# Kernel tuning notes

Measured on AMD Instinct MI355X. Metric: run time of the kernel, lower is better.

Reference implementation:

```python
import jax, jax.numpy as jnp
import numpy as np

N_CLASSES = 10   # number of distinct private-attribute labels
DIM = 16         # PCA / GMM dimension (init arg `dim`)
SIGMA = 1.0      # init arg `sigma`, cov = sigma * I


def _pca(X, k):
    # torch PCA: center, SVD of X^T, project onto first k left singular vectors
    X = X - jnp.mean(X, axis=0)
    U, _, _ = jnp.linalg.svd(X.T, full_matrices=False)  # U: [D, min(D,B)]
    return X @ U[:, :k]                                  # [B, k]


def _gmm_loss(x, labels):
    # x: [B, k] PCA-projected features, labels: [B] int class ids in [0, C)
    B = x.shape[0]
    dtype = x.dtype
    ones = jnp.ones((B,), dtype)
    counts = jax.ops.segment_sum(ones, labels, num_segments=N_CLASSES)          # [C]
    sums = jax.ops.segment_sum(x, labels, num_segments=N_CLASSES)               # [C, k]
    safe = jnp.maximum(counts, 1.0)
    means = sums / safe[:, None]                                                # [C, k]

    diff = x - means[labels]                                                    # [B, k]
    outers = diff[:, :, None] * diff[:, None, :]                                # [B, k, k]
    Ssum = jax.ops.segment_sum(outers, labels, num_segments=N_CLASSES)          # [C, k, k]
    Sigma = SIGMA * jnp.eye(DIM, dtype=dtype) + Ssum / safe[:, None, None]      # [C, k, k]

    inv = jnp.linalg.inv(Sigma)                                                 # [C, k, k]
    _, logdet = jnp.linalg.slogdet(Sigma)                                       # [C]

    # KL(N_i || N_j) = 0.5*(tr(S_j^-1 S_i) + (u_j-u_i)^T S_j^-1 (u_j-u_i) - k + logdet_j - logdet_i)
    tr = jnp.einsum('jab,iba->ij', inv, Sigma)                                  # [C, C]
    d = means[None, :, :] - means[:, None, :]                                   # d[i,j] = u_j - u_i
    maha = jnp.einsum('ija,jab,ijb->ij', d, inv, d)                             # [C, C]
    kl = 0.5 * (tr + maha - DIM + logdet[None, :] - logdet[:, None])            # [C, C]

    present = counts > 0
    W = counts[:, None] * counts[None, :]
    mask = present[:, None] & present[None, :] & ~jnp.eye(N_CLASSES, dtype=bool)
    result = jnp.sum(jnp.where(mask, kl * W, jnp.zeros_like(kl)))
    return result / (jnp.asarray(B, dtype) ** 3)


def setup_inputs() -> dict:
    key = jax.random.key(0)
    k1, k2 = jax.random.split(key)
    mu = jax.random.normal(k1, (16384, 1024), dtype=jnp.float32)
    private_attribute = jax.random.randint(k2, (16384,), 0, N_CLASSES, dtype=jnp.int32)
    return {"mu": mu, "private_attribute": private_attribute}


def reference(mu, private_attribute):
    B = mu.shape[0]
    x = mu.reshape(B, -1)          # flatten(start_dim=1)
    x = _pca(x, DIM)               # [B, DIM]
    labels = private_attribute.astype(jnp.int32)
    return _gmm_loss(x, labels)
```

## Files before the change

### kernel.cpp

```cpp
#include <hip/hip_runtime.h>
#include <math.h>

#define BN 16384
#define DN 1024

static constexpr size_t OFF_C    = 0x000000;
static constexpr size_t OFF_P    = 0x400000;
static constexpr size_t OFF_Y0   = 0x800000;
static constexpr size_t OFF_Y1   = 0x840000;
static constexpr size_t OFF_Y2   = 0x880000;
static constexpr size_t OFF_Y3   = 0x8C0000;
static constexpr size_t OFF_CQ   = 0x900000;
static constexpr size_t OFF_S64  = 0x940000;
static constexpr size_t OFF_LF   = 0x948000;
static constexpr size_t OFF_T64  = 0x950000;
static constexpr size_t OFF_V16  = 0x958000;
static constexpr size_t OFF_UT   = 0x960000;
static constexpr size_t OFF_UTT  = 0x970000;
static constexpr size_t OFF_S16  = 0x980000;
static constexpr size_t OFF_CS   = 0x980100;
static constexpr size_t OFF_TR   = 0x981100;
static constexpr size_t OFF_SCAL = 0x981200;
static constexpr size_t OFF_STAT = 0x981300;
static constexpr size_t OFF_F    = 0x990000;
static constexpr size_t OFF_M    = 0xA90000;

typedef float f32x4 __attribute__((ext_vector_type(4)));
typedef short bf16x8 __attribute__((ext_vector_type(8)));
typedef unsigned int u32x4v __attribute__((ext_vector_type(4)));

__device__ __forceinline__ float wsumf(float v){
  #pragma unroll
  for (int off=32; off; off>>=1) v += __shfl_xor(v, off, 64);
  return v;
}
__device__ __forceinline__ float wminf(float v){
  #pragma unroll
  for (int off=32; off; off>>=1) v = fminf(v, __shfl_xor(v, off, 64));
  return v;
}
__device__ __forceinline__ float wmaxf(float v){
  #pragma unroll
  for (int off=32; off; off>>=1) v = fmaxf(v, __shfl_xor(v, off, 64));
  return v;
}
__device__ __forceinline__ float lanebc(float x, int l){
  return __int_as_float(__builtin_amdgcn_readlane(__float_as_int(x), l));
}
__device__ __forceinline__ float wred64(float x){
  x += __int_as_float(__builtin_amdgcn_update_dpp(0, __float_as_int(x), 0x118, 0xf, 0xf, true));
  x += __int_as_float(__builtin_amdgcn_update_dpp(0, __float_as_int(x), 0x114, 0xf, 0xf, true));
  x += __int_as_float(__builtin_amdgcn_update_dpp(0, __float_as_int(x), 0x112, 0xf, 0xf, true));
  x += __int_as_float(__builtin_amdgcn_update_dpp(0, __float_as_int(x), 0x111, 0xf, 0xf, true));
  float s0 = lanebc(x, 15), s1 = lanebc(x, 31), s2 = lanebc(x, 47), s3 = lanebc(x, 63);
  return (s0 + s1) + (s2 + s3);
}


__global__ __launch_bounds__(256) void colsum_k(const float* __restrict__ X, float* __restrict__ cs){
  int b = blockIdx.x, t = threadIdx.x;
  float a0=0.f,a1=0.f,a2=0.f,a3=0.f;
  for (int r=0; r<256; ++r){
    const float4 v = *(const float4*)(X + (size_t)(b*256 + r)*1024 + t*4);
    a0 += v.x; a1 += v.y; a2 += v.z; a3 += v.w;
  }
  atomicAdd(&cs[t*4+0], a0); atomicAdd(&cs[t*4+1], a1);
  atomicAdd(&cs[t*4+2], a2); atomicAdd(&cs[t*4+3], a3);
}

#define SYRK_SLICES 27
#define SYRK_KCHUNK 608
#define SYRKM_SLICES 4
#define SYRKM_KCHUNK 256

__device__ __forceinline__ f32x4 mfma32(bf16x8 a, bf16x8 b, f32x4 c){
  return __builtin_amdgcn_mfma_f32_16x16x32_bf16(a, b, c, 0, 0, 0);
}

template<int KCHUNK>
__device__ __forceinline__ void syrk_mfma_body(const float* __restrict__ X, float* __restrict__ G, int KMAX){
  int bx = blockIdx.x;
  int tp = bx % 36, ks = bx / 36;
  int ti = 0, rem = tp;
  while (rem >= 8 - ti){ rem -= 8 - ti; ++ti; }
  int tj = ti + rem;
  int k0 = ks * KCHUNK;
  int kend = k0 + KCHUNK; if (kend > KMAX) kend = KMAX;

  __shared__ __attribute__((aligned(16))) unsigned int LdsT[2][3][128][20];

  int t = threadIdx.x;
  int wid = t >> 6, lane = t & 63;
  int wr = wid >> 1, wc = wid & 1;
  int lm = lane & 15;
  int lk = lane >> 4;

  f32x4 acc[4][4];
  #pragma unroll
  for (int i=0;i<4;++i)
    #pragma unroll
    for (int j=0;j<4;++j) acc[i][j] = (f32x4){0.f,0.f,0.f,0.f};

  for (int kc = k0; kc < kend; kc += 32){
    __syncthreads();
    #pragma unroll
    for (int w=0; w<4; ++w){
      int job = t + 256*w;
      int c   = job & 127;
      int pk  = job >> 7;
      int p   = pk >> 2;
      int kpg = pk & 3;
      const float* src = X + (size_t)(kc + kpg*8)*1024 + (p ? tj : ti)*128 + c;
      float e[8];
      #pragma unroll
      for (int i=0;i<8;++i) e[i] = src[(size_t)i*1024];
      unsigned hh[8]; float r2f[8]; unsigned mm[8];
      #pragma unroll
      for (int i=0;i<8;++i){
        unsigned u = __float_as_uint(e[i]);
        hh[i] = u & 0xFFFF0000u;
        float r1 = e[i] - __uint_as_float(hh[i]);
        mm[i] = __float_as_uint(r1) & 0xFFFF0000u;
        r2f[i] = r1 - __uint_as_float(mm[i]);
      }
      u32x4v hp, mp, lp;
      #pragma unroll
      for (int j=0;j<4;++j){
        hp[j] = (hh[2*j] >> 16) | hh[2*j+1];
        mp[j] = (mm[2*j] >> 16) | mm[2*j+1];
        lp[j] = (__float_as_uint(r2f[2*j]) >> 16) | (__float_as_uint(r2f[2*j+1]) & 0xFFFF0000u);
      }
      *(u32x4v*)&LdsT[p][0][c][kpg*4] = hp;
      *(u32x4v*)&LdsT[p][1][c][kpg*4] = mp;
      *(u32x4v*)&LdsT[p][2][c][kpg*4] = lp;
    }
    __syncthreads();
    bf16x8 af[3][4], bg[3][4];
    #pragma unroll
    for (int fm=0; fm<4; ++fm){
      int ca = wr*64 + fm*16 + lm;
      int cb = wc*64 + fm*16 + lm;
      #pragma unroll
      for (int tm=0; tm<3; ++tm){
        af[tm][fm] = *(const bf16x8*)&LdsT[0][tm][ca][lk*4];
        bg[tm][fm] = *(const bf16x8*)&LdsT[1][tm][cb][lk*4];
      }
    }
    #pragma unroll
    for (int fm=0; fm<4; ++fm)
      #pragma unroll
      for (int fn=0; fn<4; ++fn){
        f32x4 a = acc[fm][fn];
        a = mfma32(af[0][fm], bg[0][fn], a);
        a = mfma32(af[0][fm], bg[1][fn], a);
        a = mfma32(af[1][fm], bg[0][fn], a);
        a = mfma32(af[0][fm], bg[2][fn], a);
        a = mfma32(af[2][fm], bg[0][fn], a);
        a = mfma32(af[1][fm], bg[1][fn], a);
        acc[fm][fn] = a;
      }
  }
  #pragma unroll
  for (int fm=0; fm<4; ++fm){
    int gi = ti*128 + wr*64 + fm*16 + lk*4;
    #pragma unroll
    for (int fn=0; fn<4; ++fn){
      int gj = tj*128 + wc*64 + fn*16 + lm;
      #pragma unroll
      for (int rg=0; rg<4; ++rg)
        atomicAdd(&G[(size_t)(gi+rg)*1024 + gj], acc[fm][fn][rg]);
    }
  }
}

__global__ __launch_bounds__(256, 2) void syrk_mfma_k(const float* __restrict__ X, float* __restrict__ G){
  syrk_mfma_body<SYRK_KCHUNK>(X, G, 16384);
}
__global__ __launch_bounds__(256, 2) void syrkM_mfma_k(const float* __restrict__ X, float* __restrict__ G){
  syrk_mfma_body<SYRKM_KCHUNK>(X, G, 1024);
}

__global__ __launch_bounds__(256) void trace_k(const float* __restrict__ G, const float* __restrict__ cs,
                                               float* __restrict__ scal){
  __shared__ float red[4];
  int t = threadIdx.x;
  float s = 0.f;
  #pragma unroll
  for (int w=0; w<4; ++w){
    int i = t + 256*w;
    float d = cs[i];
    s += G[(size_t)i*1025] - d*d*(1.0f/16384.0f);
  }
  s = wsumf(s);
  if ((t & 63) == 0) red[t >> 6] = s;
  __syncthreads();
  if (t == 0){
    float trD = (red[0]+red[1]+red[2]+red[3]) * (1.0f/1024.0f);
    float c = 1.40f * trD, a = 0.25f * trD;
    scal[0] = 0.5f*(c + a);
    scal[1] = 2.0f/(c - a);
  }
}

__global__ __launch_bounds__(256) void formCChat_k(float* __restrict__ C, const float* __restrict__ cs,
                                                   const float* __restrict__ scal){
  int g = blockIdx.x*256 + threadIdx.x;
  int i = g >> 10, j = g & 1023;
  if (j < i) return;
  float mid = scal[0], ie = scal[1];
  float v = C[g] - cs[i]*cs[j]*(1.0f/16384.0f);
  float h = ie*(v - ((i==j) ? mid : 0.f));
  C[g] = h;
  C[j*1024 + i] = h;
}

__global__ __launch_bounds__(256) void formM_k(float* __restrict__ M){
  int g = blockIdx.x*256 + threadIdx.x;
  int i = g >> 10, j = g & 1023;
  if (j < i) return;
  float v = 2.f*M[g] - ((i==j) ? 1.f : 0.f);
  M[g] = v;
  M[j*1024 + i] = v;
}

__global__ void rng_k(float* __restrict__ Y){
  int idx = blockIdx.x*256 + threadIdx.x;
  unsigned h = (unsigned)idx * 2654435761u;
  h ^= h >> 16; h *= 2246822519u; h ^= h >> 13; h *= 3266489917u; h ^= h >> 16;
  Y[idx] = (float)(h & 0xFFFFFFu) * (2.0f/16777216.0f) - 1.0f;
}

__global__ __launch_bounds__(256) void mv_k(const float* __restrict__ Yt, const float* __restrict__ Cm, float* __restrict__ P){
  int bx = blockIdx.x;
  int nt = bx & 15, ks = bx >> 4;
  int n0 = nt*64, k0 = ks*64;
  __shared__ __attribute__((aligned(16))) float At[64][68];
  __shared__ __attribute__((aligned(16))) float Bt[64][68];
  int t = threadIdx.x;
  #pragma unroll
  for (int w=0; w<4; ++w){
    int job = t + 256*w;
    int m  = job >> 4, f4 = job & 15;
    float4 v = *(const float4*)(Yt + (size_t)m*1024 + k0 + f4*4);
    At[f4*4+0][m] = v.x; At[f4*4+1][m] = v.y; At[f4*4+2][m] = v.z; At[f4*4+3][m] = v.w;
    int kk = job >> 4, fn = job & 15;
    *(float4*)&Bt[kk][fn*4] = *(const float4*)(Cm + (size_t)(k0+kk)*1024 + n0 + fn*4);
  }
  __syncthreads();
  int tm = t & 15, tn = t >> 4;
  float acc[4][4];
  #pragma unroll
  for (int i=0;i<4;++i)
    #pragma unroll
    for (int j=0;j<4;++j) acc[i][j]=0.f;
  for (int kk=0; kk<64; ++kk){
    float4 a = *(const float4*)&At[kk][tm*4];
    float4 b = *(const float4*)&Bt[kk][tn*4];
    float av[4] = {a.x,a.y,a.z,a.w};
    float bv[4] = {b.x,b.y,b.z,b.w};
    #pragma unroll
    for (int i=0;i<4;++i)
      #pragma unroll
      for (int j=0;j<4;++j) acc[i][j] += av[i]*bv[j];
  }
  #pragma unroll
  for (int i=0;i<4;++i){
    float4 o; o.x=acc[i][0]; o.y=acc[i][1]; o.z=acc[i][2]; o.w=acc[i][3];
    *(float4*)(P + (size_t)(ks*64 + tm*4 + i)*1024 + n0 + tn*4) = o;
  }
}

__global__ __launch_bounds__(256) void combine_k(const float* __restrict__ P, const float* __restrict__ Tk1,
                                                 float* __restrict__ out, int mode){
  int idx = (blockIdx.x*256 + threadIdx.x)*4;
  float s0=0.f,s1=0.f,s2=0.f,s3=0.f;
  #pragma unroll
  for (int ks=0; ks<16; ++ks){
    const float4 p = *(const float4*)(P + (size_t)ks*65536 + idx);
    s0 += p.x; s1 += p.y; s2 += p.z; s3 += p.w;
  }
  float4 o;
  if (mode == 0){
    o.x=s0; o.y=s1; o.z=s2; o.w=s3;
  } else {
    const float4 t1 = *(const float4*)(Tk1 + idx);
    o.x = 2.f*s0 - t1.x; o.y = 2.f*s1 - t1.y;
    o.z = 2.f*s2 - t1.z; o.w = 2.f*s3 - t1.w;
  }
  *(float4*)(out+idx) = o;
}

__global__ __launch_bounds__(256) void gram_k(const float* __restrict__ A, const float* __restrict__ Bm, double* __restrict__ S){
  int bx = blockIdx.x;
  int i = bx >> 2, jg = bx & 3;
  __shared__ __attribute__((aligned(16))) float Ai[1024];
  __shared__ double red[16][17];
  int t = threadIdx.x;
  ((float4*)Ai)[t] = ((const float4*)(A + (size_t)i*1024))[t];
  __syncthreads();
  int jl = t >> 4, kp = t & 15;
  const float* Br = Bm + (size_t)(jg*16 + jl)*1024 + kp*64;
  const float* Ar = Ai + kp*64;
  double acc = 0.0;
  #pragma unroll 8
  for (int kk=0; kk<64; ++kk) acc += (double)Br[kk] * (double)Ar[kk];
  red[jl][kp] = acc;
  __syncthreads();
  if (t < 16){
    double s = 0.0;
    #pragma unroll
    for (int p2=0; p2<16; ++p2) s += red[t][p2];
    S[i*64 + jg*16 + t] = s;
  }
}

__global__ __launch_bounds__(64) void chol_k(const double* __restrict__ S, float* __restrict__ Lf){
  __shared__ double L[64][65];
  __shared__ double col[64];
  int t = threadIdx.x;
  for (int e=t; e<4096; e+=64) L[e>>6][e&63] = S[e];
  __syncthreads();
  for (int k=0; k<64; ++k){
    double lkk = sqrt(fmax(L[k][k], 1e-280));
    double r = 1.0/lkk;
    double ck = (t > k) ? L[t][k]*r : 0.0;
    col[t] = ck;
    if (t == k) L[k][k] = lkk;
    if (t > k)  L[t][k] = ck;
    __syncthreads();
    #pragma unroll
    for (int j=0; j<64; j+=8){
      L[t][j+0] -= ck*col[j+0];
      L[t][j+1] -= ck*col[j+1];
      L[t][j+2] -= ck*col[j+2];
      L[t][j+3] -= ck*col[j+3];
      L[t][j+4] -= ck*col[j+4];
      L[t][j+5] -= ck*col[j+5];
      L[t][j+6] -= ck*col[j+6];
      L[t][j+7] -= ck*col[j+7];
    }
    __syncthreads();
  }
  for (int e=t; e<4096; e+=64){
    int i = e >> 6, j = e & 63;
    Lf[e] = (j < i) ? (float)L[i][j] : ((j == i) ? (float)(1.0/L[i][i]) : 0.f);
  }
}

__global__ __launch_bounds__(256) void applysolve_k(const float* __restrict__ Yin, const float* __restrict__ Lf, float* __restrict__ Qout){
  int k = blockIdx.x*256 + threadIdx.x;
  float z[64];
  #pragma unroll
  for (int c=0; c<64; ++c){
    float v = Yin[(size_t)c*1024 + k];
    #pragma unroll
    for (int j=0; j<c; ++j) v -= Lf[c*64+j]*z[j];
    z[c] = v * Lf[c*64+c];
  }
  #pragma unroll
  for (int c=0; c<64; ++c) Qout[(size_t)c*1024 + k] = z[c];
}

__global__ __launch_bounds__(256) void eig16_k(const double* __restrict__ Tin, float* __restrict__ V16){
  __shared__ float A[64][65];
  __shared__ __attribute__((aligned(16))) float vS[64];
  __shared__ __attribute__((aligned(16))) float qS[64];
  __shared__ float dF[64], eF[64], e2F[64], kapS[64];
  __shared__ float lamF[16];
  __shared__ float IV[5][64][16];
  __shared__ float W[16][68];
  int t = threadIdx.x;
  int r = t & 63, p4 = t >> 6;

  for (int e=t; e<4096; e+=256){
    int i = e >> 6, j = e & 63;
    A[i][j] = (float)(0.5*(Tin[i*64+j] + Tin[(size_t)j*64+i]));
  }
  __syncthreads();

  if (p4 == 0){
    float a[64];
    #pragma unroll
    for (int j=0; j<64; ++j) a[j] = A[r][j];
    float ck = a[0];
    #pragma unroll 1
    for (int k=0; k<62; ++k){
      int kp1 = k + 1;
      bool below = (r > k);
      float ckm = below ? ck : 0.f;
      float sig = wred64(ckm*ckm);
      float x1 = __int_as_float(__builtin_amdgcn_readlane(__float_as_int(ck), kp1));
      float rr = sqrtf(sig);
      float alpha = (x1 >= 0.f) ? -rr : rr;
      float kappa = sig - alpha*x1;
      float kinv = (kappa > 1e-30f) ? 1.f/kappa : 0.f;
      float v = ckm;
      if (r == kp1) v = x1 - alpha;
      if (kinv == 0.f) v = 0.f;
      if (r == 0){ eF[k] = (kinv==0.f) ? 0.f : alpha; kapS[k] = (kinv==0.f) ? 0.f : kappa; }
      if (r == k) dF[k] = ck;
      if (below) A[r][k] = v;
      vS[r] = v;
      float p0=0.f,p1=0.f,p2=0.f,p3=0.f;
      #pragma unroll
      for (int j=0; j<64; j+=4){
        const float4 vb = *(const float4*)&vS[j];
        p0 += a[j+0]*vb.x; p1 += a[j+1]*vb.y;
        p2 += a[j+2]*vb.z; p3 += a[j+3]*vb.w;
      }
      float pf = (p0+p1)+(p2+p3);
      float pi = below ? pf*kinv : 0.f;
      float vp = wred64(v*pi);
      float Kc = vp*0.5f*kinv;
      float q = below ? (pi - Kc*v) : 0.f;
      qS[r] = q;
      float ckn = 0.f;
      #pragma unroll
      for (int j=0; j<64; j+=4){
        const float4 vb = *(const float4*)&vS[j];
        const float4 qb = *(const float4*)&qS[j];
        a[j+0] -= v*qb.x + q*vb.x;
        a[j+1] -= v*qb.y + q*vb.y;
        a[j+2] -= v*qb.z + q*vb.z;
        a[j+3] -= v*qb.w + q*vb.w;
        if (j+0 == kp1) ckn = a[j+0];
        if (j+1 == kp1) ckn = a[j+1];
        if (j+2 == kp1) ckn = a[j+2];
        if (j+3 == kp1) ckn = a[j+3];
      }
      ck = ckn;
    }
    if (r == 62) dF[62] = ck;
    if (r == 63){ eF[62] = ck; dF[63] = a[63]; }
    if (r == 0){ eF[63] = 0.f; kapS[62] = 0.f; kapS[63] = 0.f; }
  }
  __syncthreads();
  if (t < 64) e2F[t] = eF[t]*eF[t];
  __syncthreads();

  float em1 = (r > 0) ? fabsf(eF[r-1]) : 0.f;
  float ep  = fabsf(eF[r]);
  float glo = wminf(dF[r] - em1 - ep);
  float ghi = wmaxf(dF[r] + em1 + ep);
  float span = ghi - glo + 1.f;
  float lo = glo - 0.001f*span, hi = ghi + 0.001f*span;

  int eidx = t >> 4, g = t & 15;
  int m = 48 + eidx;
  for (int it=0; it<7; ++it){
    float x = lo + (hi - lo)*((float)(g+1)*(1.0f/17.0f));
    float qq = dF[0] - x;
    int c = (qq < 0.f) ? 1 : 0;
    #pragma unroll
    for (int j=1; j<64; ++j){
      float aq = fabsf(qq);
      float qs = (aq < 1e-10f) ? ((qq < 0.f) ? -1e-10f : 1e-10f) : qq;
      qq = dF[j] - x - e2F[j-1]*__builtin_amdgcn_rcpf(qs);
      c += (qq < 0.f) ? 1 : 0;
    }
    float cl = (c <= m) ? x : -3.4e38f;
    float ch = (c >  m) ? x :  3.4e38f;
    #pragma unroll
    for (int off=1; off<16; off<<=1){
      cl = fmaxf(cl, __shfl_xor(cl, off, 64));
      ch = fminf(ch, __shfl_xor(ch, off, 64));
    }
    lo = fmaxf(lo, cl);
    hi = fminf(hi, ch);
  }
  if (g == 0) lamF[eidx] = 0.5f*(lo + hi);
  __syncthreads();

  if (t < 16){
    float lam = lamF[t];
    const float PIVF = 1e-6f;
    #pragma unroll 4
    for (int i=0; i<64; ++i){
      unsigned hsh = (unsigned)(i*131 + t*1009 + 7);
      hsh ^= hsh >> 13; hsh *= 2654435761u; hsh ^= hsh >> 16;
      IV[4][i][t] = (float)(hsh & 0xFFFF) * (1.5f/65536.0f) + 0.25f;
    }
    unsigned long long piv = 0ull;
    float dcur = dF[0] - lam;
    float ducur = eF[0];
    for (int i=0; i<63; ++i){
      float dli = eF[i];
      float dnext = dF[i+1] - lam;
      float eip1 = (i < 62) ? eF[i+1] : 0.f;
      bool sw = fabsf(dcur) < fabsf(dli);
      float dd = dcur;
      if (fabsf(dd) < PIVF) dd = (dd < 0.f) ? -PIVF : PIVF;
      float f = sw ? (dcur*__builtin_amdgcn_rcpf(dli)) : (dli*__builtin_amdgcn_rcpf(dd));
      float ddst = sw ? dli : dd;
      float dust = sw ? dnext : ducur;
      float du2  = sw ? eip1 : 0.f;
      float dnew = sw ? (ducur - f*dnext) : (dnext - f*ducur);
      float dunew= sw ? (-f*eip1) : eip1;
      if (sw) piv |= (1ull << i);
      IV[0][i][t] = f;
      float dc = ddst; if (fabsf(dc) < PIVF) dc = (dc < 0.f) ? -PIVF : PIVF;
      IV[1][i][t] = __builtin_amdgcn_rcpf(dc);
      IV[2][i][t] = dust;
      IV[3][i][t] = du2;
      dcur = dnew; ducur = dunew;
    }
    { float dc = dcur; if (fabsf(dc) < PIVF) dc = (dc < 0.f) ? -PIVF : PIVF; IV[1][63][t] = __builtin_amdgcn_rcpf(dc); }
    float ss = 0.f;
    #pragma unroll 1
    for (int iter=0; iter<2; ++iter){
      float scale = (iter == 0) ? 1.f : rsqrtf(fmaxf(ss, 1e-30f));
      float b = IV[4][0][t]*scale;
      #pragma unroll 7
      for (int i=0; i<63; ++i){
        float bn = IV[4][i+1][t]*scale;
        float f = IV[0][i][t];
        bool sw = (piv >> i) & 1ull;
        float keep = sw ? bn : b;
        float bnew = (sw ? b : bn) - f*keep;
        IV[4][i][t] = keep;
        b = bnew;
      }
      ss = 0.f;
      float x1v = b * IV[1][63][t];
      IV[4][63][t] = x1v; ss += x1v*x1v;
      float x0v = (IV[4][62][t] - IV[2][62][t]*x1v) * IV[1][62][t];
      IV[4][62][t] = x0v; ss += x0v*x0v;
      float xp1 = x0v, xp2 = x1v;
      #pragma unroll 7
      for (int i=61; i>=0; --i){
        float xi = (IV[4][i][t] - IV[2][i][t]*xp1 - IV[3][i][t]*xp2) * IV[1][i][t];
        IV[4][i][t] = xi; ss += xi*xi;
        xp2 = xp1; xp1 = xi;
      }
    }
    #pragma unroll 4
    for (int i=0; i<64; ++i) W[t][i] = IV[4][i][t];
  }
  __syncthreads();

  for (int c=0; c<16; ++c){
    float wi = (t < 64) ? W[c][t] : 0.f;
    float s2 = wred64(wi*wi);
    float rn = rsqrtf(fmaxf(s2, 1e-30f));
    wi *= rn;
    if (t < 64) W[c][t] = wi;
    __syncthreads();
    for (int c2=c+1; c2<16; ++c2){
      float w2 = (t < 64) ? W[c2][t] : 0.f;
      float d2 = wred64(wi*w2);
      if (t < 64) W[c2][t] -= d2*wi;
    }
    __syncthreads();
  }

  int cL = (p4 << 2) + (r >> 4);
  int part = r & 15;
  for (int k=61; k>=0; --k){
    float kpd = kapS[k];
    if (kpd == 0.f) continue;
    float invk = 1.f/kpd;
    float vv[4];
    float ps = 0.f;
    #pragma unroll
    for (int mm=0; mm<4; ++mm){
      int i = part*4 + mm;
      vv[mm] = (i > k) ? A[i][k] : 0.f;
      ps += vv[mm]*W[cL][i];
    }
    ps += __shfl_xor(ps, 1, 64);
    ps += __shfl_xor(ps, 2, 64);
    ps += __shfl_xor(ps, 4, 64);
    ps += __shfl_xor(ps, 8, 64);
    float sc = ps * invk;
    #pragma unroll
    for (int mm=0; mm<4; ++mm){
      int i = part*4 + mm;
      W[cL][i] -= vv[mm]*sc;
    }
  }
  __syncthreads();

  for (int e=t; e<1024; e+=256){
    int j = e >> 4, c = e & 15;
    V16[e] = W[c][j];
  }
}

__global__ __launch_bounds__(256) void buildUt_k(const float* __restrict__ V16,
                                                 const float* __restrict__ Qt, float* __restrict__ Ut, float* __restrict__ UtT){
  int bx = blockIdx.x;
  int c = bx & 15, kc = bx >> 4;
  int k = kc*256 + threadIdx.x;
  float acc = 0.f;
  #pragma unroll
  for (int j=0; j<64; ++j) acc += V16[j*16 + c] * Qt[(size_t)j*1024 + k];
  Ut[(size_t)c*1024 + k] = acc;
  UtT[(size_t)k*16 + c] = acc;
}

__global__ void s16_k(const float* __restrict__ cs, const float* __restrict__ Ut, float* __restrict__ s16){
  __shared__ float red[16][17];
  int t = threadIdx.x;
  int c = t & 15, part = t >> 4;
  float acc = 0.f;
  for (int d=0; d<64; ++d) acc += cs[part*64 + d] * Ut[(size_t)c*1024 + part*64 + d];
  red[c][part] = acc;
  __syncthreads();
  if (t < 16){
    float s = 0.f;
    #pragma unroll
    for (int p2=0; p2<16; ++p2) s += red[t][p2];
    s16[t] = s * (1.0f/16384.0f);
  }
}

__global__ __launch_bounds__(256) void proj_k(const float* __restrict__ X, const float* __restrict__ UtT,
                                              const float* __restrict__ s16, float* __restrict__ F){
  int r0 = blockIdx.x * 64;
  int t = threadIdx.x;
  __shared__ __attribute__((aligned(16))) float uts[16384];
  #pragma unroll
  for (int w=0; w<16; ++w)
    ((float4*)uts)[t + 256*w] = ((const float4*)UtT)[t + 256*w];
  __syncthreads();
  int row = t & 63, kp = t >> 6;
  const float* xr = X + (size_t)(r0 + row)*1024 + kp*256;
  const float* ut = uts + kp*256*16;
  float acc[16];
  #pragma unroll
  for (int c=0;c<16;++c) acc[c] = 0.f;
  for (int dd=0; dd<256; dd+=4){
    float4 xv4 = *(const float4*)(xr + dd);
    float xv[4] = {xv4.x, xv4.y, xv4.z, xv4.w};
    #pragma unroll
    for (int u=0; u<4; ++u)
      #pragma unroll
      for (int c=0;c<16;++c) acc[c] += xv[u] * ut[(dd+u)*16 + c];
  }
  __shared__ float part[4][64][16];
  #pragma unroll
  for (int c=0;c<16;++c) part[kp][row][c] = acc[c];
  __syncthreads();
  int cq = t >> 6;
  #pragma unroll
  for (int ccx=0; ccx<4; ++ccx){
    int c = cq*4 + ccx;
    float v = part[0][row][c] + part[1][row][c] + part[2][row][c] + part[3][row][c] - s16[c];
    F[(size_t)(r0 + row)*16 + c] = v;
  }
}

__global__ __launch_bounds__(256) void stats_k(const float* __restrict__ F, const int* __restrict__ lbl, float* __restrict__ SG){
  __shared__ float st[10][154];
  int t = threadIdx.x;
  for (int e=t; e<1540; e+=256) st[e/154][e%154] = 0.f;
  __syncthreads();
  int r = blockIdx.x*256 + t;
  float f[16];
  #pragma unroll
  for (int w=0; w<4; ++w){
    float4 v = *(const float4*)(F + (size_t)r*16 + w*4);
    f[w*4+0]=v.x; f[w*4+1]=v.y; f[w*4+2]=v.z; f[w*4+3]=v.w;
  }
  int c = lbl[r];
  if ((unsigned)c < 10u){
    float* bs = &st[c][0];
    atomicAdd(&bs[0], 1.f);
    #pragma unroll
    for (int a=0;a<16;++a) atomicAdd(&bs[1+a], f[a]);
    int sidx = 17;
    #pragma unroll
    for (int a=0;a<16;++a)
      #pragma unroll
      for (int b2=a;b2<16;++b2) atomicAdd(&bs[sidx++], f[a]*f[b2]);
  }
  __syncthreads();
  for (int e=t; e<1530; e+=256) atomicAdd(&SG[e], st[e/153][e%153]);
}

__global__ __launch_bounds__(256) void final_k(const float* __restrict__ SG, float* __restrict__ out){
  __shared__ double cnt[10], safe[10], ldet[10];
  __shared__ double mean[10][16];
  __shared__ double Sig[10][16][16];
  __shared__ double Inv[10][16][16];
  __shared__ double red[128];
  int t = threadIdx.x;
  if (t < 10){
    double c0 = (double)SG[t*153];
    cnt[t] = c0; safe[t] = (c0 > 0.0) ? c0 : 1.0;
  }
  __syncthreads();
  for (int e=t; e<160; e+=256){
    int c = e >> 4, a = e & 15;
    mean[c][a] = (double)SG[c*153 + 1 + a] / safe[c];
  }
  __syncthreads();
  for (int e=t; e<2560; e+=256){
    int c = e >> 8, ab = e & 255, a = ab >> 4, b2 = ab & 15;
    int lo = a < b2 ? a : b2, hi = a < b2 ? b2 : a;
    int ti = lo*(33 - lo)/2 + (hi - lo);
    Sig[c][a][b2] = (double)SG[c*153 + 17 + ti]/safe[c] - mean[c][a]*mean[c][b2] + ((a==b2)?1.0:0.0);
  }
  __syncthreads();
  if (t < 10){
    for (int a=0;a<16;++a)
      for (int b2=0;b2<16;++b2) Inv[t][a][b2] = Sig[t][a][b2];
    double ld2 = 0.0;
    for (int k=0;k<16;++k){
      double v = Inv[t][k][k];
      for (int j=0;j<k;++j) v -= Inv[t][k][j]*Inv[t][k][j];
      v = fmax(v, 1e-280);
      double lkk = sqrt(v);
      Inv[t][k][k] = lkk; ld2 += log(lkk);
      for (int i=k+1;i<16;++i){
        double w = Inv[t][i][k];
        for (int j=0;j<k;++j) w -= Inv[t][i][j]*Inv[t][k][j];
        Inv[t][i][k] = w / lkk;
      }
    }
    ldet[t] = 2.0*ld2;
    for (int j=0;j<16;++j){
      double dj = 1.0 / Inv[t][j][j];
      Inv[t][j][j] = dj;
      for (int i=j+1;i<16;++i){
        double ssum = Inv[t][i][j]*dj;
        for (int k=j+1;k<i;++k) ssum += Inv[t][i][k]*Inv[t][k][j];
        Inv[t][i][j] = -ssum / Inv[t][i][i];
      }
    }
    double dg[16];
    #pragma unroll
    for (int a=0;a<16;++a){
      double s2 = 0.0;
      for (int k=a;k<16;++k){ double x = Inv[t][k][a]; s2 += x*x; }
      dg[a] = s2;
    }
    for (int a=0;a<16;++a)
      for (int b2=a+1;b2<16;++b2){
        double s2 = 0.0;
        for (int k=b2;k<16;++k) s2 += Inv[t][k][a]*Inv[t][k][b2];
        Inv[t][a][b2] = s2;
      }
    for (int a=0;a<16;++a) Inv[t][a][a] = dg[a];
    for (int a=0;a<16;++a)
      for (int b2=a+1;b2<16;++b2) Inv[t][b2][a] = Inv[t][a][b2];
  }
  __syncthreads();
  double contrib = 0.0;
  if (t < 100){
    int i = t/10, j = t%10;
    if (i != j && cnt[i] > 0.0 && cnt[j] > 0.0){
      double tr = 0.0;
      for (int a=0;a<16;++a)
        for (int b2=0;b2<16;++b2) tr += Inv[j][a][b2]*Sig[i][b2][a];
      double dm[16];
      #pragma unroll
      for (int a=0;a<16;++a) dm[a] = mean[j][a] - mean[i][a];
      double mah = 0.0;
      for (int a=0;a<16;++a){
        double rs = 0.0;
        for (int b2=0;b2<16;++b2) rs += Inv[j][a][b2]*dm[b2];
        mah += dm[a]*rs;
      }
      double kl = 0.5*(tr + mah - 16.0 + ldet[j] - ldet[i]);
      contrib = kl * cnt[i]*cnt[j];
    }
  }
  if (t < 128) red[t] = contrib;
  __syncthreads();
  for (int off=64; off>0; off >>= 1){
    if (t < off) red[t] += red[t+off];
    __syncthreads();
  }
  if (t == 0) out[0] = (float)(red[0] / (16384.0*16384.0*16384.0));
}

extern "C" void kernel_launch(void* const* d_in, const int* in_sizes, int n_in,
                              void* d_out, int out_size, void* d_ws, size_t ws_size,
                              hipStream_t stream){
  (void)in_sizes; (void)n_in; (void)out_size; (void)ws_size;
  const float* X  = (const float*)d_in[0];
  const int* lbl  = (const int*)d_in[1];
  char* ws = (char*)d_ws;
  float*  C    = (float*)(ws + OFF_C);
  float*  Mm   = (float*)(ws + OFF_M);
  float*  P    = (float*)(ws + OFF_P);
  float*  Y0   = (float*)(ws + OFF_Y0);
  float*  Y1   = (float*)(ws + OFF_Y1);
  float*  Y2   = (float*)(ws + OFF_Y2);
  float*  Y3   = (float*)(ws + OFF_Y3);
  float*  CQ   = (float*)(ws + OFF_CQ);
  double* S64  = (double*)(ws + OFF_S64);
  float*  LF   = (float*)(ws + OFF_LF);
  double* T64  = (double*)(ws + OFF_T64);
  float*  V16  = (float*)(ws + OFF_V16);
  float*  UT   = (float*)(ws + OFF_UT);
  float*  UTT  = (float*)(ws + OFF_UTT);
  float*  S16  = (float*)(ws + OFF_S16);
  float*  CS   = (float*)(ws + OFF_CS);
  float*  SCAL = (float*)(ws + OFF_SCAL);
  float*  STAT = (float*)(ws + OFF_STAT);
  float*  F    = (float*)(ws + OFF_F);
  float*  OUT  = (float*)d_out;

  hipMemsetAsync(C, 0, 4*1024*1024, stream);
  hipMemsetAsync(Mm, 0, 4*1024*1024, stream);
  hipMemsetAsync(ws + OFF_CS, 0, 12800, stream);

  colsum_k<<<64, 256, 0, stream>>>(X, CS);
  syrk_mfma_k<<<36*SYRK_SLICES, 256, 0, stream>>>(X, C);
  trace_k<<<1, 256, 0, stream>>>(C, CS, SCAL);
  formCChat_k<<<4096, 256, 0, stream>>>(C, CS, SCAL);
  syrkM_mfma_k<<<36*SYRKM_SLICES, 256, 0, stream>>>(C, Mm);
  formM_k<<<4096, 256, 0, stream>>>(Mm);
  hipMemsetAsync(P, 0, 4*1024*1024, stream);
  syrkM_mfma_k<<<36*SYRKM_SLICES, 256, 0, stream>>>(Mm, P);
  formM_k<<<4096, 256, 0, stream>>>(P);
  hipMemsetAsync(C, 0, 4*1024*1024, stream);
  syrkM_mfma_k<<<36*SYRKM_SLICES, 256, 0, stream>>>(P, C);
  formM_k<<<4096, 256, 0, stream>>>(C);
  rng_k<<<256, 256, 0, stream>>>(Y0);

  auto cheb2 = [&](float* U, float* Wb, float* Ob){
    mv_k<<<256, 256, 0, stream>>>(U, C, P);
    combine_k<<<64, 256, 0, stream>>>(P, U, Wb, 0);
    mv_k<<<256, 256, 0, stream>>>(Wb, C, P);
    combine_k<<<64, 256, 0, stream>>>(P, U, Ob, 1);
  };
  auto cholqr = [&](float* Yin, float* Qout){
    gram_k<<<256, 256, 0, stream>>>(Yin, Yin, S64);
    chol_k<<<1, 64, 0, stream>>>(S64, LF);
    applysolve_k<<<4, 256, 0, stream>>>(Yin, LF, Qout);
  };

  cheb2(Y0, Y1, Y2);
  cholqr(Y2, Y0);
  cheb2(Y0, Y1, Y2);
  cholqr(Y2, Y1);
  cholqr(Y1, Y3);

  mv_k<<<256, 256, 0, stream>>>(Y3, Mm, P);
  combine_k<<<64, 256, 0, stream>>>(P, Y3, CQ, 0);
  gram_k<<<256, 256, 0, stream>>>(Y3, CQ, T64);
  eig16_k<<<1, 256, 0, stream>>>(T64, V16);
  buildUt_k<<<64, 256, 0, stream>>>(V16, Y3, UT, UTT);

  s16_k<<<1, 256, 0, stream>>>(CS, UT, S16);
  proj_k<<<256, 256, 0, stream>>>(X, UTT, S16, F);
  stats_k<<<64, 256, 0, stream>>>(F, lbl, STAT);
  final_k<<<1, 256, 0, stream>>>(STAT, OUT);
}
```

Measured before the change: 1.129 ms.

## Fuse split-K matvec with combine, widen colsum grid, use lane broadcasts in tridiagonalization

Replaces the split-K mv_k plus combine_k pair with one mvc_k kernel. Each block loops over the full K dimension and writes the final (optionally Chebyshev-combined) result, which removes the partial-sum buffer traffic and a launch per product. The colsum kernel now uses 256 blocks of 64 rows instead of 64 blocks of 256. The eig16 Householder loop swaps its shared-memory vector exchange for readlane broadcasts and skips column blocks already eliminated. The fused matvec launches only 64 blocks, so it may underuse the GPU.

```diff
diff --git a/kernel.cpp b/kernel.cpp
--- a/kernel.cpp
+++ b/kernel.cpp
@@ -60,8 +60,8 @@
 __global__ __launch_bounds__(256) void colsum_k(const float* __restrict__ X, float* __restrict__ cs){
   int b = blockIdx.x, t = threadIdx.x;
   float a0=0.f,a1=0.f,a2=0.f,a3=0.f;
-  for (int r=0; r<256; ++r){
-    const float4 v = *(const float4*)(X + (size_t)(b*256 + r)*1024 + t*4);
+  for (int r=0; r<64; ++r){
+    const float4 v = *(const float4*)(X + (size_t)(b*64 + r)*1024 + t*4);
     a0 += v.x; a1 += v.y; a2 += v.z; a3 += v.w;
   }
   atomicAdd(&cs[t*4+0], a0); atomicAdd(&cs[t*4+1], a1);
@@ -230,64 +230,47 @@
   Y[idx] = (float)(h & 0xFFFFFFu) * (2.0f/16777216.0f) - 1.0f;
 }
 
-__global__ __launch_bounds__(256) void mv_k(const float* __restrict__ Yt, const float* __restrict__ Cm, float* __restrict__ P){
+__global__ __launch_bounds__(256) void mvc_k(const float* __restrict__ U, const float* __restrict__ Mz,
+                                             const float* __restrict__ Pv, float* __restrict__ out, int mode){
   int bx = blockIdx.x;
-  int nt = bx & 15, ks = bx >> 4;
-  int n0 = nt*64, k0 = ks*64;
-  __shared__ __attribute__((aligned(16))) float At[64][68];
+  int rg = bx >> 4, nt = bx & 15;
+  int m0 = rg*16, n0 = nt*64;
+  __shared__ __attribute__((aligned(16))) float At[64][17];
   __shared__ __attribute__((aligned(16))) float Bt[64][68];
   int t = threadIdx.x;
-  #pragma unroll
-  for (int w=0; w<4; ++w){
-    int job = t + 256*w;
-    int m  = job >> 4, f4 = job & 15;
-    float4 v = *(const float4*)(Yt + (size_t)m*1024 + k0 + f4*4);
-    At[f4*4+0][m] = v.x; At[f4*4+1][m] = v.y; At[f4*4+2][m] = v.z; At[f4*4+3][m] = v.w;
-    int kk = job >> 4, fn = job & 15;
-    *(float4*)&Bt[kk][fn*4] = *(const float4*)(Cm + (size_t)(k0+kk)*1024 + n0 + fn*4);
-  }
-  __syncthreads();
   int tm = t & 15, tn = t >> 4;
-  float acc[4][4];
-  #pragma unroll
-  for (int i=0;i<4;++i)
-    #pragma unroll
-    for (int j=0;j<4;++j) acc[i][j]=0.f;
-  for (int kk=0; kk<64; ++kk){
-    float4 a = *(const float4*)&At[kk][tm*4];
-    float4 b = *(const float4*)&Bt[kk][tn*4];
-    float av[4] = {a.x,a.y,a.z,a.w};
-    float bv[4] = {b.x,b.y,b.z,b.w};
-    #pragma unroll
-    for (int i=0;i<4;++i)
-      #pragma unroll
-      for (int j=0;j<4;++j) acc[i][j] += av[i]*bv[j];
-  }
-  #pragma unroll
-  for (int i=0;i<4;++i){
-    float4 o; o.x=acc[i][0]; o.y=acc[i][1]; o.z=acc[i][2]; o.w=acc[i][3];
-    *(float4*)(P + (size_t)(ks*64 + tm*4 + i)*1024 + n0 + tn*4) = o;
-  }
-}
-
-__global__ __launch_bounds__(256) void combine_k(const float* __restrict__ P, const float* __restrict__ Tk1,
-                                                 float* __restrict__ out, int mode){
-  int idx = (blockIdx.x*256 + threadIdx.x)*4;
-  float s0=0.f,s1=0.f,s2=0.f,s3=0.f;
-  #pragma unroll
-  for (int ks=0; ks<16; ++ks){
-    const float4 p = *(const float4*)(P + (size_t)ks*65536 + idx);
-    s0 += p.x; s1 += p.y; s2 += p.z; s3 += p.w;
-  }
-  float4 o;
+  float acc[4] = {0.f,0.f,0.f,0.f};
+  for (int kc = 0; kc < 1024; kc += 64){
+    __syncthreads();
+    {
+      int m = t & 15, k4 = t >> 4;
+      float4 uv = *(const float4*)(U + (size_t)(m0+m)*1024 + kc + k4*4);
+      At[k4*4+0][m] = uv.x; At[k4*4+1][m] = uv.y; At[k4*4+2][m] = uv.z; At[k4*4+3][m] = uv.w;
+    }
+    #pragma unroll
+    for (int w=0; w<4; ++w){
+      int job = t + 256*w;
+      int k = job >> 4, n4 = job & 15;
+      *(float4*)&Bt[k][n4*4] = *(const float4*)(Mz + (size_t)(kc+k)*1024 + n0 + n4*4);
+    }
+    __syncthreads();
+    #pragma unroll 8
+    for (int kk=0; kk<64; ++kk){
+      float av = At[kk][tm];
+      const float4 b = *(const float4*)&Bt[kk][tn*4];
+      acc[0] += av*b.x; acc[1] += av*b.y; acc[2] += av*b.z; acc[3] += av*b.w;
+    }
+  }
+  size_t o = (size_t)(m0+tm)*1024 + n0 + tn*4;
+  float4 ov;
   if (mode == 0){
-    o.x=s0; o.y=s1; o.z=s2; o.w=s3;
+    ov.x=acc[0]; ov.y=acc[1]; ov.z=acc[2]; ov.w=acc[3];
   } else {
-    const float4 t1 = *(const float4*)(Tk1 + idx);
-    o.x = 2.f*s0 - t1.x; o.y = 2.f*s1 - t1.y;
-    o.z = 2.f*s2 - t1.z; o.w = 2.f*s3 - t1.w;
-  }
-  *(float4*)(out+idx) = o;
+    const float4 pv = *(const float4*)(Pv + o);
+    ov.x = 2.f*acc[0]-pv.x; ov.y = 2.f*acc[1]-pv.y;
+    ov.z = 2.f*acc[2]-pv.z; ov.w = 2.f*acc[3]-pv.w;
+  }
+  *(float4*)(out+o) = ov;
 }
 
 __global__ __launch_bounds__(256) void gram_k(const float* __restrict__ A, const float* __restrict__ Bm, double* __restrict__ S){
@@ -363,8 +346,6 @@
 
 __global__ __launch_bounds__(256) void eig16_k(const double* __restrict__ Tin, float* __restrict__ V16){
   __shared__ float A[64][65];
-  __shared__ __attribute__((aligned(16))) float vS[64];
-  __shared__ __attribute__((aligned(16))) float qS[64];
   __shared__ float dF[64], eF[64], e2F[64], kapS[64];
   __shared__ float lamF[16];
   __shared__ float IV[5][64][16];
@@ -386,10 +367,11 @@
     #pragma unroll 1
     for (int k=0; k<62; ++k){
       int kp1 = k + 1;
+      int jb0 = k >> 4;
       bool below = (r > k);
       float ckm = below ? ck : 0.f;
       float sig = wred64(ckm*ckm);
-      float x1 = __int_as_float(__builtin_amdgcn_readlane(__float_as_int(ck), kp1));
+      float x1 = lanebc(ck, kp1);
       float rr = sqrtf(sig);
       float alpha = (x1 >= 0.f) ? -rr : rr;
       float kappa = sig - alpha*x1;
@@ -400,33 +382,35 @@
       if (r == 0){ eF[k] = (kinv==0.f) ? 0.f : alpha; kapS[k] = (kinv==0.f) ? 0.f : kappa; }
       if (r == k) dF[k] = ck;
       if (below) A[r][k] = v;
-      vS[r] = v;
-      float p0=0.f,p1=0.f,p2=0.f,p3=0.f;
-      #pragma unroll
-      for (int j=0; j<64; j+=4){
-        const float4 vb = *(const float4*)&vS[j];
-        p0 += a[j+0]*vb.x; p1 += a[j+1]*vb.y;
-        p2 += a[j+2]*vb.z; p3 += a[j+3]*vb.w;
-      }
-      float pf = (p0+p1)+(p2+p3);
+      float pf = 0.f;
+      #pragma unroll
+      for (int jb=0; jb<4; ++jb){
+        if (jb >= jb0){
+          #pragma unroll
+          for (int jj=0; jj<16; ++jj){
+            int j = jb*16 + jj;
+            pf += a[j]*lanebc(v, j);
+          }
+        }
+      }
       float pi = below ? pf*kinv : 0.f;
       float vp = wred64(v*pi);
       float Kc = vp*0.5f*kinv;
       float q = below ? (pi - Kc*v) : 0.f;
-      qS[r] = q;
       float ckn = 0.f;
       #pragma unroll
-      for (int j=0; j<64; j+=4){
-        const float4 vb = *(const float4*)&vS[j];
-        const float4 qb = *(const float4*)&qS[j];
-        a[j+0] -= v*qb.x + q*vb.x;
-        a[j+1] -= v*qb.y + q*vb.y;
-        a[j+2] -= v*qb.z + q*vb.z;
-        a[j+3] -= v*qb.w + q*vb.w;
-        if (j+0 == kp1) ckn = a[j+0];
-        if (j+1 == kp1) ckn = a[j+1];
-        if (j+2 == kp1) ckn = a[j+2];
-        if (j+3 == kp1) ckn = a[j+3];
+      for (int jb=0; jb<4; ++jb){
+        if (jb >= jb0){
+          #pragma unroll
+          for (int jj=0; jj<16; ++jj){
+            int j = jb*16 + jj;
+            float vj = lanebc(v, j);
+            float qj = lanebc(q, j);
+            float an = a[j] - (v*qj + q*vj);
+            a[j] = an;
+            ckn = (j == kp1) ? an : ckn;
+          }
+        }
       }
       ck = ckn;
     }
@@ -807,7 +791,7 @@
   hipMemsetAsync(Mm, 0, 4*1024*1024, stream);
   hipMemsetAsync(ws + OFF_CS, 0, 12800, stream);
 
-  colsum_k<<<64, 256, 0, stream>>>(X, CS);
+  colsum_k<<<256, 256, 0, stream>>>(X, CS);
   syrk_mfma_k<<<36*SYRK_SLICES, 256, 0, stream>>>(X, C);
   trace_k<<<1, 256, 0, stream>>>(C, CS, SCAL);
   formCChat_k<<<4096, 256, 0, stream>>>(C, CS, SCAL);
@@ -822,10 +806,8 @@
   rng_k<<<256, 256, 0, stream>>>(Y0);
 
   auto cheb2 = [&](float* U, float* Wb, float* Ob){
-    mv_k<<<256, 256, 0, stream>>>(U, C, P);
-    combine_k<<<64, 256, 0, stream>>>(P, U, Wb, 0);
-    mv_k<<<256, 256, 0, stream>>>(Wb, C, P);
-    combine_k<<<64, 256, 0, stream>>>(P, U, Ob, 1);
+    mvc_k<<<64, 256, 0, stream>>>(U, C, U, Wb, 0);
+    mvc_k<<<64, 256, 0, stream>>>(Wb, C, U, Ob, 1);
   };
   auto cholqr = [&](float* Yin, float* Qout){
     gram_k<<<256, 256, 0, stream>>>(Yin, Yin, S64);
@@ -839,8 +821,7 @@
   cholqr(Y2, Y1);
   cholqr(Y1, Y3);
 
-  mv_k<<<256, 256, 0, stream>>>(Y3, Mm, P);
-  combine_k<<<64, 256, 0, stream>>>(P, Y3, CQ, 0);
+  mvc_k<<<64, 256, 0, stream>>>(Y3, Mm, Y3, CQ, 0);
   gram_k<<<256, 256, 0, stream>>>(Y3, CQ, T64);
   eig16_k<<<1, 256, 0, stream>>>(T64, V16);
   buildUt_k<<<64, 256, 0, stream>>>(V16, Y3, UT, UTT);
```

New measurement: 1.224 ms. +8.4%, slower.

## Swizzle SYRK LDS layout, use lane broadcasts in tridiagonalization, widen colsum grid

Applied to the files above, without the earlier changes.

Three unrelated changes. The column-sum kernel now runs 256 blocks of 64 rows each instead of 64 blocks of 256 rows, which spreads the reads over more CUs at the cost of more atomics. The SYRK kernel XOR-swizzles the 16-byte chunk position within each LDS row to reduce bank conflicts. The 64x64 Householder tridiagonalization replaces its LDS vector staging with readlane broadcasts and skips column blocks already eliminated, which removes shared-memory traffic from the serial eigen stage but emits many scalar readlane instructions.

```diff
diff --git a/kernel.cpp b/kernel.cpp
--- a/kernel.cpp
+++ b/kernel.cpp
@@ -60,8 +60,8 @@
 __global__ __launch_bounds__(256) void colsum_k(const float* __restrict__ X, float* __restrict__ cs){
   int b = blockIdx.x, t = threadIdx.x;
   float a0=0.f,a1=0.f,a2=0.f,a3=0.f;
-  for (int r=0; r<256; ++r){
-    const float4 v = *(const float4*)(X + (size_t)(b*256 + r)*1024 + t*4);
+  for (int r=0; r<64; ++r){
+    const float4 v = *(const float4*)(X + (size_t)(b*64 + r)*1024 + t*4);
     a0 += v.x; a1 += v.y; a2 += v.z; a3 += v.w;
   }
   atomicAdd(&cs[t*4+0], a0); atomicAdd(&cs[t*4+1], a1);
@@ -75,6 +75,10 @@
 
 __device__ __forceinline__ f32x4 mfma32(bf16x8 a, bf16x8 b, f32x4 c){
   return __builtin_amdgcn_mfma_f32_16x16x32_bf16(a, b, c, 0, 0, 0);
+}
+
+__device__ __forceinline__ int lds_woff(int c, int chunk){
+  return c*20 + (((chunk ^ ((c>>3)&3)) & 3) << 2);
 }
 
 template<int KCHUNK>
@@ -130,9 +134,10 @@
         mp[j] = (mm[2*j] >> 16) | mm[2*j+1];
         lp[j] = (__float_as_uint(r2f[2*j]) >> 16) | (__float_as_uint(r2f[2*j+1]) & 0xFFFF0000u);
       }
-      *(u32x4v*)&LdsT[p][0][c][kpg*4] = hp;
-      *(u32x4v*)&LdsT[p][1][c][kpg*4] = mp;
-      *(u32x4v*)&LdsT[p][2][c][kpg*4] = lp;
+      int wo = lds_woff(c, kpg);
+      *(u32x4v*)(&LdsT[p][0][0][0] + wo) = hp;
+      *(u32x4v*)(&LdsT[p][1][0][0] + wo) = mp;
+      *(u32x4v*)(&LdsT[p][2][0][0] + wo) = lp;
     }
     __syncthreads();
     bf16x8 af[3][4], bg[3][4];
@@ -140,10 +145,12 @@
     for (int fm=0; fm<4; ++fm){
       int ca = wr*64 + fm*16 + lm;
       int cb = wc*64 + fm*16 + lm;
+      int woa = lds_woff(ca, lk);
+      int wob = lds_woff(cb, lk);
       #pragma unroll
       for (int tm=0; tm<3; ++tm){
-        af[tm][fm] = *(const bf16x8*)&LdsT[0][tm][ca][lk*4];
-        bg[tm][fm] = *(const bf16x8*)&LdsT[1][tm][cb][lk*4];
+        af[tm][fm] = *(const bf16x8*)(&LdsT[0][tm][0][0] + woa);
+        bg[tm][fm] = *(const bf16x8*)(&LdsT[1][tm][0][0] + wob);
       }
     }
     #pragma unroll
@@ -363,8 +370,6 @@
 
 __global__ __launch_bounds__(256) void eig16_k(const double* __restrict__ Tin, float* __restrict__ V16){
   __shared__ float A[64][65];
-  __shared__ __attribute__((aligned(16))) float vS[64];
-  __shared__ __attribute__((aligned(16))) float qS[64];
   __shared__ float dF[64], eF[64], e2F[64], kapS[64];
   __shared__ float lamF[16];
   __shared__ float IV[5][64][16];
@@ -386,10 +391,11 @@
     #pragma unroll 1
     for (int k=0; k<62; ++k){
       int kp1 = k + 1;
+      int jb0 = k >> 4;
       bool below = (r > k);
       float ckm = below ? ck : 0.f;
       float sig = wred64(ckm*ckm);
-      float x1 = __int_as_float(__builtin_amdgcn_readlane(__float_as_int(ck), kp1));
+      float x1 = lanebc(ck, kp1);
       float rr = sqrtf(sig);
       float alpha = (x1 >= 0.f) ? -rr : rr;
       float kappa = sig - alpha*x1;
@@ -400,33 +406,35 @@
       if (r == 0){ eF[k] = (kinv==0.f) ? 0.f : alpha; kapS[k] = (kinv==0.f) ? 0.f : kappa; }
       if (r == k) dF[k] = ck;
       if (below) A[r][k] = v;
-      vS[r] = v;
-      float p0=0.f,p1=0.f,p2=0.f,p3=0.f;
-      #pragma unroll
-      for (int j=0; j<64; j+=4){
-        const float4 vb = *(const float4*)&vS[j];
-        p0 += a[j+0]*vb.x; p1 += a[j+1]*vb.y;
-        p2 += a[j+2]*vb.z; p3 += a[j+3]*vb.w;
-      }
-      float pf = (p0+p1)+(p2+p3);
+      float pf = 0.f;
+      #pragma unroll
+      for (int jb=0; jb<4; ++jb){
+        if (jb >= jb0){
+          #pragma unroll
+          for (int jj=0; jj<16; ++jj){
+            int j = jb*16 + jj;
+            pf += a[j]*lanebc(v, j);
+          }
+        }
+      }
       float pi = below ? pf*kinv : 0.f;
       float vp = wred64(v*pi);
       float Kc = vp*0.5f*kinv;
       float q = below ? (pi - Kc*v) : 0.f;
-      qS[r] = q;
       float ckn = 0.f;
       #pragma unroll
-      for (int j=0; j<64; j+=4){
-        const float4 vb = *(const float4*)&vS[j];
-        const float4 qb = *(const float4*)&qS[j];
-        a[j+0] -= v*qb.x + q*vb.x;
-        a[j+1] -= v*qb.y + q*vb.y;
-        a[j+2] -= v*qb.z + q*vb.z;
-        a[j+3] -= v*qb.w + q*vb.w;
-        if (j+0 == kp1) ckn = a[j+0];
-        if (j+1 == kp1) ckn = a[j+1];
-        if (j+2 == kp1) ckn = a[j+2];
-        if (j+3 == kp1) ckn = a[j+3];
+      for (int jb=0; jb<4; ++jb){
+        if (jb >= jb0){
+          #pragma unroll
+          for (int jj=0; jj<16; ++jj){
+            int j = jb*16 + jj;
+            float vj = lanebc(v, j);
+            float qj = lanebc(q, j);
+            float an = a[j] - (v*qj + q*vj);
+            a[j] = an;
+            ckn = (j == kp1) ? an : ckn;
+          }
+        }
       }
       ck = ckn;
     }
@@ -807,7 +815,7 @@
   hipMemsetAsync(Mm, 0, 4*1024*1024, stream);
   hipMemsetAsync(ws + OFF_CS, 0, 12800, stream);
 
-  colsum_k<<<64, 256, 0, stream>>>(X, CS);
+  colsum_k<<<256, 256, 0, stream>>>(X, CS);
   syrk_mfma_k<<<36*SYRK_SLICES, 256, 0, stream>>>(X, C);
   trace_k<<<1, 256, 0, stream>>>(C, CS, SCAL);
   formCChat_k<<<4096, 256, 0, stream>>>(C, CS, SCAL);
```

Result: no change. 1.129 ms (-0.0%).
